# Optimization experiments

Hardware: AMD Instinct MI355X
Metric: run time of the kernel (lower is better)

The kernel has to match this reference:

```python
import jax, jax.numpy as jnp
import numpy as np

B, S, D, H = 4, 1024, 1024, 16
HD = D // H  # head_dim = 64


def setup_inputs() -> dict:
    key = jax.random.key(0)
    ks = jax.random.split(key, 18)
    s = 0.02
    return {
        "x": jax.random.normal(ks[0], (B, S, D), jnp.float32),
        "trust_scores": jax.random.uniform(ks[1], (B, S), jnp.float32),
        "mask": jax.random.randint(ks[2], (B, S), 0, 2).astype(jnp.int32),
        # Linear weights stored as (in, out); torch does x @ W.T + b, equivalent here.
        "Wq": jax.random.normal(ks[3], (D, D), jnp.float32) * s,
        "bq": jnp.zeros((D,), jnp.float32),
        "Wk": jax.random.normal(ks[4], (D, D), jnp.float32) * s,
        "bk": jnp.zeros((D,), jnp.float32),
        "Wv": jax.random.normal(ks[5], (D, D), jnp.float32) * s,
        "bv": jnp.zeros((D,), jnp.float32),
        "Wtp": jax.random.normal(ks[6], (1, HD), jnp.float32) * s,
        "btp": jnp.zeros((HD,), jnp.float32),
        "Wg": jax.random.normal(ks[7], (D + 1, D), jnp.float32) * s,
        "bg": jnp.zeros((D,), jnp.float32),
        "Wo": jax.random.normal(ks[8], (D, D), jnp.float32) * s,
        "bo": jnp.zeros((D,), jnp.float32),
    }


def reference(x, trust_scores, mask, Wq, bq, Wk, bk, Wv, bv, Wtp, btp, Wg, bg, Wo, bo):
    b, s, d = x.shape
    hd = Wtp.shape[1]
    h = d // hd
    # QKV projections -> [b, h, s, hd]
    q = (x @ Wq + bq).reshape(b, s, h, hd).transpose(0, 2, 1, 3)
    k = (x @ Wk + bk).reshape(b, s, h, hd).transpose(0, 2, 1, 3)
    v = (x @ Wv + bv).reshape(b, s, h, hd).transpose(0, 2, 1, 3)
    scores = jnp.einsum("bhqd,bhkd->bhqk", q, k) / jnp.sqrt(jnp.float32(hd))
    # Trust affinity bias: project scalar trust -> head_dim, outer-product + sigmoid.
    trust_proj = trust_scores[:, :, None] @ Wtp + btp  # [b, s, hd]
    trust_aff = jax.nn.sigmoid(jnp.einsum("bqd,bkd->bqk", trust_proj, trust_proj))
    scores = scores + 0.1 * trust_aff[:, None, :, :]  # broadcast over heads
    # Mask applies along the QUERY axis (mask.unsqueeze(1).unsqueeze(-1) in torch).
    scores = jnp.where(mask[:, None, :, None] == 0, jnp.float32(-1e9), scores)
    attn = jax.nn.softmax(scores, axis=-1)  # [b, h, s, s]
    attended = jnp.einsum("bhqk,bhkd->bhqd", attn, v)
    attended = attended.transpose(0, 2, 1, 3).reshape(b, s, d)
    # Trust gate: sigmoid(Linear([attended, trust])) elementwise gate.
    gate_in = jnp.concatenate([attended, trust_scores[:, :, None]], axis=-1)
    gate = jax.nn.sigmoid(gate_in @ Wg + bg)
    attended = attended * gate
    output = attended @ Wo + bo
    return (output, attn)
```

## Files before the change

### kernel.cpp

```cpp
#include <hip/hip_runtime.h>
#include <math.h>

#define BB 4
#define SS 1024
#define DD 1024
#define HH 16
#define HDD 64
#define MTOT (BB*SS)
#define MB (1024*1024)

typedef float  f32x4  __attribute__((ext_vector_type(4)));
typedef __bf16 bf16x8 __attribute__((ext_vector_type(8)));
typedef unsigned short u16;

__device__ __forceinline__ unsigned short f2bf(float f) {
    union { float f; unsigned u; } v; v.f = f;
    unsigned r = v.u + 0x7FFFu + ((v.u >> 16) & 1u);
    return (unsigned short)(r >> 16);
}
__device__ __forceinline__ float bf2f(unsigned short u) {
    union { unsigned u; float f; } v; v.u = ((unsigned)u) << 16;
    return v.f;
}
__device__ __forceinline__ f32x4 mfma16(bf16x8 a, bf16x8 b, f32x4 c) {
    return __builtin_amdgcn_mfma_f32_16x16x32_bf16(a, b, c, 0, 0, 0);
}
__device__ __forceinline__ void gload16(const void* g, void* l) {
    __builtin_amdgcn_global_load_lds(
        (const __attribute__((address_space(1))) void*)g,
        (__attribute__((address_space(3))) void*)l, 16, 0, 0);
}
__device__ __forceinline__ void lds_fence() {
    asm volatile("s_waitcnt lgkmcnt(0)" ::: "memory");
    __builtin_amdgcn_sched_barrier(0);
}

__global__ void split_kernel(const float* __restrict__ in, u16* __restrict__ hi,
                             u16* __restrict__ lo, int n4)
{
    for (int i = blockIdx.x*blockDim.x + threadIdx.x; i < n4; i += gridDim.x*blockDim.x) {
        f32x4 v = ((const f32x4*)in)[i];
        ushort4 h4, l4;
        h4.x = f2bf(v[0]); l4.x = f2bf(v[0] - bf2f(h4.x));
        h4.y = f2bf(v[1]); l4.y = f2bf(v[1] - bf2f(h4.y));
        h4.z = f2bf(v[2]); l4.z = f2bf(v[2] - bf2f(h4.z));
        h4.w = f2bf(v[3]); l4.w = f2bf(v[3] - bf2f(h4.w));
        ((ushort4*)hi)[i] = h4; ((ushort4*)lo)[i] = l4;
    }
}

__global__ __launch_bounds__(256)
void tsplit5_kernel(const float* W0, u16* h0,
                    const float* W1, u16* h1,
                    const float* W2, u16* h2,
                    const float* W3, u16* h3,
                    const float* W4, u16* h4, u16* l4T)
{
    const float* W; u16* hT; u16* lT = nullptr;
    switch (blockIdx.z) {
        case 0: W = W0; hT = h0; break;
        case 1: W = W1; hT = h1; break;
        case 2: W = W2; hT = h2; break;
        case 3: W = W3; hT = h3; break;
        default: W = W4; hT = h4; lT = l4T; break;
    }
    __shared__ float tile[64][65];
    const int t  = threadIdx.x;
    const int k0 = blockIdx.y * 64, n0 = blockIdx.x * 64;
    const int r  = t >> 4, c4 = (t & 15) * 4;
    #pragma unroll
    for (int rr = 0; rr < 4; ++rr) {
        const int k = r + rr*16;
        f32x4 v = *(const f32x4*)&W[(size_t)(k0 + k)*1024 + n0 + c4];
        tile[k][c4+0] = v[0]; tile[k][c4+1] = v[1]; tile[k][c4+2] = v[2]; tile[k][c4+3] = v[3];
    }
    __syncthreads();
    #pragma unroll
    for (int rr = 0; rr < 4; ++rr) {
        const int nl = r + rr*16;
        ushort4 hh, ll;
        {
            float v;
            v = tile[c4+0][nl]; hh.x = f2bf(v); ll.x = f2bf(v - bf2f(hh.x));
            v = tile[c4+1][nl]; hh.y = f2bf(v); ll.y = f2bf(v - bf2f(hh.y));
            v = tile[c4+2][nl]; hh.z = f2bf(v); ll.z = f2bf(v - bf2f(hh.z));
            v = tile[c4+3][nl]; hh.w = f2bf(v); ll.w = f2bf(v - bf2f(hh.w));
        }
        *(ushort4*)&hT[(size_t)(n0 + nl)*1024 + k0 + c4] = hh;
        if (lT) *(ushort4*)&lT[(size_t)(n0 + nl)*1024 + k0 + c4] = ll;
    }
}

__global__ void tconst_kernel(const float* __restrict__ Wtp, const float* __restrict__ btp,
                              float* __restrict__ out3)
{
    const int l = threadIdx.x;
    const float w = Wtp[l], b = btp[l];
    float a = w*w, m = w*b, c = b*b;
    #pragma unroll
    for (int s = 32; s; s >>= 1) {
        a += __shfl_down(a, s);
        m += __shfl_down(m, s);
        c += __shfl_down(c, s);
    }
    if (l == 0) { out3[0] = a; out3[1] = m; out3[2] = c; }
}

__global__ __launch_bounds__(256)
void tbias_kernel(const float* __restrict__ trust, const float* __restrict__ tconst,
                  u16* __restrict__ T)
{
    const int b = blockIdx.y;
    const int q = blockIdx.x;
    const float tq = trust[b*SS + q];
    const float c1 = tconst[0], c2 = tconst[1], c3 = tconst[2];
    const int k0 = threadIdx.x * 4;
    f32x4 tk = *(const f32x4*)&trust[b*SS + k0];
    ushort4 o;
    #pragma unroll
    for (int j = 0; j < 4; ++j) {
        const float ta = c1*tq*tk[j] + c2*(tq + tk[j]) + c3;
        const float v  = 0.1f/(1.f + __expf(-ta));
        ((u16*)&o)[j] = f2bf(v);
    }
    *(ushort4*)&T[((size_t)b*SS + q)*SS + k0] = o;
}

template<int MODE, int PASSES>
__global__ __launch_bounds__(256)
void mgemm(const u16* __restrict__ Ah, const u16* __restrict__ Al,
           const u16* __restrict__ Bh, const u16* __restrict__ Bl,
           const float* __restrict__ bias,
           float* __restrict__ outF, u16* __restrict__ outH, u16* __restrict__ outL,
           int M, int N,
           const float* __restrict__ trust, const float* __restrict__ wlast,
           const u16* __restrict__ attH, const u16* __restrict__ attL)
{
    constexpr int NT   = (PASSES == 3) ? 4 : (PASSES == 2) ? 3 : 2;
    constexpr int BIDX = (PASSES == 1) ? 1 : 2;
    __shared__ u16 lds[2][NT][128*64];

    const int t    = threadIdx.x;
    const int lane = t & 63, wave = t >> 6;
    const int l15  = lane & 15, l4 = lane >> 4;
    const int wr   = wave >> 1, wc = wave & 1;
    const int w64  = wave << 6;
    const int m0   = blockIdx.y * 128, n0 = blockIdx.x * 128;

    const u16* srcs[NT];
    srcs[0] = Ah + (size_t)m0*1024;
    if (PASSES >= 2) srcs[1] = Al + (size_t)m0*1024;
    srcs[BIDX] = Bh + (size_t)n0*1024;
    if (PASSES == 3) srcs[3] = Bl + (size_t)n0*1024;

    f32x4 acc[4][4];
    #pragma unroll
    for (int i = 0; i < 4; ++i)
        #pragma unroll
        for (int j = 0; j < 4; ++j) acc[i][j] = (f32x4){0.f,0.f,0.f,0.f};

#define STAGE(BUF, KOFF) do {                                                  \
    _Pragma("unroll")                                                          \
    for (int tl_ = 0; tl_ < NT; ++tl_) {                                       \
        _Pragma("unroll")                                                      \
        for (int it_ = 0; it_ < 4; ++it_) {                                    \
            const int idx_ = it_*256 + t;                                      \
            const int row_ = idx_ >> 3;                                        \
            const int c_   = (idx_ & 7) ^ (row_ & 7);                          \
            gload16(srcs[tl_] + (KOFF) + (size_t)row_*1024 + c_*8,             \
                    &lds[BUF][tl_][(it_*256 + w64)*8]);                        \
        }                                                                      \
    }                                                                          \
} while(0)

#define COMPUTE(BUF) do {                                                      \
    _Pragma("unroll")                                                          \
    for (int kk_ = 0; kk_ < 2; ++kk_) {                                        \
        const int cb_ = (kk_<<2) + l4;                                         \
        bf16x8 ah_[4], al_[4];                                                 \
        _Pragma("unroll")                                                      \
        for (int i_ = 0; i_ < 4; ++i_) {                                       \
            const int row_ = (wr<<6) + (i_<<4) + l15;                          \
            const int off_ = (row_<<6) + ((cb_ ^ (row_&7)) << 3);              \
            ah_[i_] = *(const bf16x8*)&lds[BUF][0][off_];                      \
            if (PASSES >= 2) al_[i_] = *(const bf16x8*)&lds[BUF][1][off_];     \
        }                                                                      \
        _Pragma("unroll")                                                      \
        for (int j_ = 0; j_ < 4; ++j_) {                                       \
            const int row_ = (wc<<6) + (j_<<4) + l15;                          \
            const int off_ = (row_<<6) + ((cb_ ^ (row_&7)) << 3);              \
            bf16x8 bh_ = *(const bf16x8*)&lds[BUF][BIDX][off_];                \
            bf16x8 bl_;                                                        \
            if (PASSES == 3) bl_ = *(const bf16x8*)&lds[BUF][3][off_];         \
            _Pragma("unroll")                                                  \
            for (int i_ = 0; i_ < 4; ++i_) {                                   \
                acc[i_][j_] = mfma16(ah_[i_], bh_, acc[i_][j_]);               \
                if (PASSES == 3) acc[i_][j_] = mfma16(ah_[i_], bl_, acc[i_][j_]); \
                if (PASSES >= 2) acc[i_][j_] = mfma16(al_[i_], bh_, acc[i_][j_]); \
            }                                                                  \
        }                                                                      \
    }                                                                          \
} while(0)

    STAGE(0, 0);
    __syncthreads();
    int cur = 0;
    for (int s = 0; s < 15; ++s) {
        if (cur == 0) STAGE(1, (s+1)*64);
        else          STAGE(0, (s+1)*64);
        COMPUTE(cur);
        __syncthreads();
        cur ^= 1;
    }
    COMPUTE(cur);
#undef STAGE
#undef COMPUTE

    #pragma unroll
    for (int i = 0; i < 4; ++i)
        #pragma unroll
        for (int j = 0; j < 4; ++j)
            #pragma unroll
            for (int r = 0; r < 4; ++r) {
                const int m = m0 + (wr<<6) + (i<<4) + (l4<<2) + r;
                const int n = n0 + (wc<<6) + (j<<4) + l15;
                const float v = acc[i][j][r];
                if (MODE == 0) {
                    outF[(size_t)m*N + n] = v + bias[n];
                } else if (MODE == 2) {
                    outH[(size_t)m*N + n] = f2bf(v + bias[n]);
                } else if (MODE == 4) {
                    const size_t blk = (((size_t)((m >> 10)*16 + (n >> 6)))*64
                                        + ((m >> 4) & 63))*1024;
                    outH[blk + ((n & 63) >> 3)*128 + (m & 15)*8 + (n & 7)]
                        = f2bf(v + bias[n]);
                } else if (MODE == 5) {
                    const size_t blk = ((((size_t)((n >> 10)*16 + (m >> 6)))*32
                                        + ((n & 1023) >> 5))*4 + ((m & 63) >> 4))*512;
                    outH[blk + ((n & 31) >> 3)*128 + (m & 15)*8 + (n & 7)]
                        = f2bf(v + bias[m]);
                } else {
                    const float pre = v + bias[n] + trust[m]*wlast[n];
                    const float g = 1.f/(1.f + __expf(-pre));
                    const float att = bf2f(attH[(size_t)m*N + n]) + bf2f(attL[(size_t)m*N + n]);
                    const float gated = att*g;
                    const unsigned short hb = f2bf(gated);
                    outH[(size_t)m*N + n] = hb;
                    outL[(size_t)m*N + n] = f2bf(gated - bf2f(hb));
                }
            }
}

__global__ __launch_bounds__(512, 4)
void attn_kernel(const u16* __restrict__ Qb, const u16* __restrict__ Kf,
                 const u16* __restrict__ Vf, const u16* __restrict__ T,
                 const int* __restrict__ mask,
                 float* __restrict__ attnOut, u16* __restrict__ attH, u16* __restrict__ attL)
{
    __shared__ float Pw[8][16*68 + 16];
    __shared__ float redA[8][16];
    __shared__ float redB[8][16];

    const int t    = threadIdx.x;
    const int lane = t & 63, wave = t >> 6;
    const int l15  = lane & 15, l4 = lane >> 4;

    const int bid  = blockIdx.x;
    const int xcd  = bid & 7;
    const int idx0 = bid >> 3;
    const int q0   = (idx0 & 63) * 16;
    const int Pn   = ((idx0 >> 6) << 3) + xcd;
    const int h    = Pn & 15;
    const int b    = Pn >> 4;

    float* myP = Pw[wave];

    int mrow[4];
    #pragma unroll
    for (int r = 0; r < 4; ++r) mrow[r] = mask[b*SS + q0 + l4*4 + r];

    const u16* Qp = Qb + ((size_t)(b*SS + q0 + l15))*DD + h*HDD + l4*8;
    bf16x8 qf0 = *(const bf16x8*)Qp;
    bf16x8 qf1 = *(const bf16x8*)(Qp + 32);

    f32x4 sacc[8];
    #pragma unroll
    for (int tt = 0; tt < 8; ++tt) sacc[tt] = (f32x4){0.f,0.f,0.f,0.f};

    const u16* Kbase = Kf + (((size_t)(b*16 + h))*64 + wave*8)*1024 + l4*128 + l15*8;
    #pragma unroll
    for (int tt = 0; tt < 8; ++tt) {
        bf16x8 kf0 = *(const bf16x8*)(Kbase + tt*1024);
        bf16x8 kf1 = *(const bf16x8*)(Kbase + tt*1024 + 512);
        sacc[tt] = mfma16(qf0, kf0, sacc[tt]);
        sacc[tt] = mfma16(qf1, kf1, sacc[tt]);
    }

    const u16* Tb = T + ((size_t)b*SS + q0 + l4*4)*SS + wave*128 + l15;
    float mx[4] = {-3e38f, -3e38f, -3e38f, -3e38f};
    #pragma unroll
    for (int tt = 0; tt < 8; ++tt) {
        #pragma unroll
        for (int r = 0; r < 4; ++r) {
            const float bias = bf2f(Tb[(size_t)r*SS + tt*16]);
            float s = sacc[tt][r]*0.125f + bias;
            s = mrow[r] ? s : -1e9f;
            sacc[tt][r] = s;
            mx[r] = fmaxf(mx[r], s);
        }
    }
    #pragma unroll
    for (int r = 0; r < 4; ++r)
        #pragma unroll
        for (int xm = 1; xm < 16; xm <<= 1) mx[r] = fmaxf(mx[r], __shfl_xor(mx[r], xm));
    if (l15 == 0) {
        #pragma unroll
        for (int r = 0; r < 4; ++r) redA[wave][l4*4 + r] = mx[r];
    }
    __syncthreads();

    float mxa[4];
    #pragma unroll
    for (int r = 0; r < 4; ++r) {
        const int row = l4*4 + r;
        float m = redA[0][row];
        #pragma unroll
        for (int w = 1; w < 8; ++w) m = fmaxf(m, redA[w][row]);
        mxa[r] = m;
    }

    float sum[4] = {0.f, 0.f, 0.f, 0.f};
    #pragma unroll
    for (int tt = 0; tt < 8; ++tt)
        #pragma unroll
        for (int r = 0; r < 4; ++r) {
            const float p = __expf(sacc[tt][r] - mxa[r]);
            sacc[tt][r] = p;
            sum[r] += p;
        }
    #pragma unroll
    for (int r = 0; r < 4; ++r)
        #pragma unroll
        for (int xm = 1; xm < 16; xm <<= 1) sum[r] += __shfl_xor(sum[r], xm);
    if (l15 == 0) {
        #pragma unroll
        for (int r = 0; r < 4; ++r) redB[wave][l4*4 + r] = sum[r];
    }
    __syncthreads();

    float inv4[4];
    #pragma unroll
    for (int r = 0; r < 4; ++r) {
        const int row = l4*4 + r;
        float s8 = 0.f;
        #pragma unroll
        for (int w = 0; w < 8; ++w) s8 += redB[w][row];
        inv4[r] = 1.f / s8;
    }
    float wiv4[4];
    #pragma unroll
    for (int it = 0; it < 4; ++it) {
        const int row = it*4 + l4;
        float s8 = 0.f;
        #pragma unroll
        for (int w = 0; w < 8; ++w) s8 += redB[w][row];
        wiv4[it] = 1.f / s8;
    }

    float* gBase = attnOut + (((size_t)(b*HH + h))*SS + q0)*SS + wave*128;
    f32x4 pv[4];
    #pragma unroll
    for (int nt = 0; nt < 4; ++nt) pv[nt] = (f32x4){0.f,0.f,0.f,0.f};

    #pragma unroll
    for (int half = 0; half < 2; ++half) {
        #pragma unroll
        for (int t2 = 0; t2 < 4; ++t2)
            #pragma unroll
            for (int r = 0; r < 4; ++r)
                myP[(l4*4 + r)*68 + t2*16 + l15] = sacc[half*4 + t2][r];
        lds_fence();

        #pragma unroll
        for (int it = 0; it < 4; ++it) {
            const int row = it*4 + l4;
            f32x4 v = *(f32x4*)&myP[row*68 + l15*4];
            v *= wiv4[it];
            *(f32x4*)&gBase[(size_t)row*SS + half*64 + l15*4] = v;
        }

        #pragma unroll
        for (int kg = 0; kg < 2; ++kg) {
            const int c0 = kg*32 + l4*8;
            f32x4 a0 = *(f32x4*)&myP[l15*68 + c0];
            f32x4 a1 = *(f32x4*)&myP[l15*68 + c0 + 4];
            bf16x8 af;
            af[0] = (__bf16)a0[0]; af[1] = (__bf16)a0[1]; af[2] = (__bf16)a0[2]; af[3] = (__bf16)a0[3];
            af[4] = (__bf16)a1[0]; af[5] = (__bf16)a1[1]; af[6] = (__bf16)a1[2]; af[7] = (__bf16)a1[3];
            const int kc = wave*4 + half*2 + kg;
            const u16* Vp = Vf + (((size_t)(b*16 + h))*32 + kc)*2048 + l4*128 + l15*8;
            #pragma unroll
            for (int nt = 0; nt < 4; ++nt) {
                bf16x8 bf = *(const bf16x8*)(Vp + nt*512);
                pv[nt] = mfma16(af, bf, pv[nt]);
            }
        }
        lds_fence();
    }

    #pragma unroll
    for (int nt = 0; nt < 4; ++nt)
        #pragma unroll
        for (int r = 0; r < 4; ++r)
            myP[(l4*4 + r)*64 + nt*16 + l15] = pv[nt][r] * inv4[r];
    __syncthreads();

    {
        const int q = t >> 5, d0 = (t & 31)*2;
        float sx = 0.f, sy = 0.f;
        #pragma unroll
        for (int w = 0; w < 8; ++w) {
            float2 v = *(float2*)&Pw[w][q*64 + d0];
            sx += v.x; sy += v.y;
        }
        const size_t off = ((size_t)(b*SS + q0 + q))*DD + h*HDD + d0;
        const unsigned short h0 = f2bf(sx), h1 = f2bf(sy);
        ushort2 hh = {h0, h1};
        ushort2 ll = {f2bf(sx - bf2f(h0)), f2bf(sy - bf2f(h1))};
        *(ushort2*)&attH[off] = hh;
        *(ushort2*)&attL[off] = ll;
    }
}

extern "C" void kernel_launch(void* const* d_in, const int* in_sizes, int n_in,
                              void* d_out, int out_size, void* d_ws, size_t ws_size,
                              hipStream_t stream) {
    const float* x     = (const float*)d_in[0];
    const float* trust = (const float*)d_in[1];
    const int*   mask  = (const int*)  d_in[2];
    const float* Wq    = (const float*)d_in[3];
    const float* bq    = (const float*)d_in[4];
    const float* Wk    = (const float*)d_in[5];
    const float* bk    = (const float*)d_in[6];
    const float* Wv    = (const float*)d_in[7];
    const float* bv    = (const float*)d_in[8];
    const float* Wtp   = (const float*)d_in[9];
    const float* btp   = (const float*)d_in[10];
    const float* Wg    = (const float*)d_in[11];
    const float* bg    = (const float*)d_in[12];
    const float* Wo    = (const float*)d_in[13];
    const float* bo    = (const float*)d_in[14];

    float* out     = (float*)d_out;
    float* attnOut = out + (size_t)MTOT * DD;

    char* ws = (char*)d_ws;
    u16* xh   = (u16*)(ws + (size_t)0*MB);
    u16* xl   = (u16*)(ws + (size_t)8*MB);
    u16* WqTh = (u16*)(ws + (size_t)16*MB);
    u16* WkTh = (u16*)(ws + (size_t)18*MB);
    u16* WvTh = (u16*)(ws + (size_t)20*MB);
    u16* WgTh = (u16*)(ws + (size_t)22*MB);
    u16* WoTh = (u16*)(ws + (size_t)24*MB);
    u16* WoTl = (u16*)(ws + (size_t)26*MB);
    u16* Qbf  = (u16*)(ws + (size_t)28*MB);
    u16* Kfb  = (u16*)(ws + (size_t)36*MB);
    u16* Vfb  = (u16*)(ws + (size_t)44*MB);
    u16* Tb   = (u16*)(ws + (size_t)52*MB);
    float* tconst = (float*)(ws + (size_t)60*MB);
    u16* attH = xh;
    u16* attL = xl;
    u16* Gh   = Qbf;
    u16* Gl   = Kfb;

    const dim3 blk(256);

    tconst_kernel<<<1, 64, 0, stream>>>(Wtp, btp, tconst);
    tbias_kernel<<<dim3(SS, BB), blk, 0, stream>>>(trust, tconst, Tb);
    split_kernel<<<2048, blk, 0, stream>>>(x, xh, xl, MTOT*DD/4);
    tsplit5_kernel<<<dim3(16, 16, 5), blk, 0, stream>>>(
        Wq, WqTh, Wk, WkTh, Wv, WvTh, Wg, WgTh, Wo, WoTh, WoTl);

    mgemm<2,2><<<dim3(DD/128, MTOT/128), blk, 0, stream>>>(
        xh, xl, WqTh, nullptr, bq, nullptr, Qbf, nullptr, MTOT, DD,
        nullptr, nullptr, nullptr, nullptr);
    mgemm<4,2><<<dim3(DD/128, MTOT/128), blk, 0, stream>>>(
        xh, xl, WkTh, nullptr, bk, nullptr, Kfb, nullptr, MTOT, DD,
        nullptr, nullptr, nullptr, nullptr);
    mgemm<5,1><<<dim3(MTOT/128, DD/128), blk, 0, stream>>>(
        WvTh, nullptr, xh, nullptr, bv, nullptr, Vfb, nullptr, DD, MTOT,
        nullptr, nullptr, nullptr, nullptr);

    attn_kernel<<<dim3(4096), dim3(512), 0, stream>>>(
        Qbf, Kfb, Vfb, Tb, mask, attnOut, attH, attL);

    mgemm<1,1><<<dim3(DD/128, MTOT/128), blk, 0, stream>>>(
        attH, nullptr, WgTh, nullptr, bg, nullptr, Gh, Gl, MTOT, DD,
        trust, Wg + (size_t)DD*DD, attH, attL);
    mgemm<0,3><<<dim3(DD/128, MTOT/128), blk, 0, stream>>>(
        Gh, Gl, WoTh, WoTl, bo, out, nullptr, nullptr, MTOT, DD,
        nullptr, nullptr, nullptr, nullptr);
}
```

Baseline: 247.4 us.

## Fuse Q/K projections into one single-pass GEMM and tile trust-bias layout

```diff
diff --git a/kernel.cpp b/kernel.cpp
--- a/kernel.cpp
+++ b/kernel.cpp
@@ -40,12 +40,15 @@
 {
     for (int i = blockIdx.x*blockDim.x + threadIdx.x; i < n4; i += gridDim.x*blockDim.x) {
         f32x4 v = ((const f32x4*)in)[i];
-        ushort4 h4, l4;
-        h4.x = f2bf(v[0]); l4.x = f2bf(v[0] - bf2f(h4.x));
-        h4.y = f2bf(v[1]); l4.y = f2bf(v[1] - bf2f(h4.y));
-        h4.z = f2bf(v[2]); l4.z = f2bf(v[2] - bf2f(h4.z));
-        h4.w = f2bf(v[3]); l4.w = f2bf(v[3] - bf2f(h4.w));
-        ((ushort4*)hi)[i] = h4; ((ushort4*)lo)[i] = l4;
+        ushort4 h4;
+        h4.x = f2bf(v[0]); h4.y = f2bf(v[1]); h4.z = f2bf(v[2]); h4.w = f2bf(v[3]);
+        ((ushort4*)hi)[i] = h4;
+        if (lo) {
+            ushort4 l4v;
+            l4v.x = f2bf(v[0] - bf2f(h4.x)); l4v.y = f2bf(v[1] - bf2f(h4.y));
+            l4v.z = f2bf(v[2] - bf2f(h4.z)); l4v.w = f2bf(v[3] - bf2f(h4.w));
+            ((ushort4*)lo)[i] = l4v;
+        }
     }
 }
 
@@ -108,22 +111,28 @@
 
 __global__ __launch_bounds__(256)
 void tbias_kernel(const float* __restrict__ trust, const float* __restrict__ tconst,
-                  u16* __restrict__ T)
+                  u16* __restrict__ T2)
 {
-    const int b = blockIdx.y;
-    const int q = blockIdx.x;
-    const float tq = trust[b*SS + q];
+    const int qt = blockIdx.x;
+    const int b  = blockIdx.y;
+    const int t  = threadIdx.x;
+    const int lane = t & 63, grp = t >> 6;
+    const int l15 = lane & 15, l4 = lane >> 4;
     const float c1 = tconst[0], c2 = tconst[1], c3 = tconst[2];
-    const int k0 = threadIdx.x * 4;
-    f32x4 tk = *(const f32x4*)&trust[b*SS + k0];
-    ushort4 o;
-    #pragma unroll
-    for (int j = 0; j < 4; ++j) {
-        const float ta = c1*tq*tk[j] + c2*(tq + tk[j]) + c3;
-        const float v  = 0.1f/(1.f + __expf(-ta));
-        ((u16*)&o)[j] = f2bf(v);
-    }
-    *(ushort4*)&T[((size_t)b*SS + q)*SS + k0] = o;
+    float tq[4];
+    #pragma unroll
+    for (int r = 0; r < 4; ++r) tq[r] = trust[b*SS + qt*16 + l4*4 + r];
+    for (int kt2 = 0; kt2 < 16; ++kt2) {
+        const int kt = grp*16 + kt2;
+        const float tk = trust[b*SS + kt*16 + l15];
+        ushort4 o;
+        #pragma unroll
+        for (int r = 0; r < 4; ++r) {
+            const float ta = c1*tq[r]*tk + c2*(tq[r] + tk) + c3;
+            ((u16*)&o)[r] = f2bf(0.1f/(1.f + __expf(-ta)));
+        }
+        *(ushort4*)&T2[((((size_t)b*64 + qt)*64 + kt)*64 + lane)*4] = o;
+    }
 }
 
 template<int MODE, int PASSES>
@@ -150,7 +159,12 @@
     const u16* srcs[NT];
     srcs[0] = Ah + (size_t)m0*1024;
     if (PASSES >= 2) srcs[1] = Al + (size_t)m0*1024;
-    srcs[BIDX] = Bh + (size_t)n0*1024;
+    if (MODE == 6) {
+        srcs[BIDX] = (n0 < 1024) ? Bh + (size_t)n0*1024
+                                 : Bl + (size_t)(n0 - 1024)*1024;
+    } else {
+        srcs[BIDX] = Bh + (size_t)n0*1024;
+    }
     if (PASSES == 3) srcs[3] = Bl + (size_t)n0*1024;
 
     f32x4 acc[4][4];
@@ -239,6 +253,16 @@
                                         + ((n & 1023) >> 5))*4 + ((m & 63) >> 4))*512;
                     outH[blk + ((n & 31) >> 3)*128 + (m & 15)*8 + (n & 7)]
                         = f2bf(v + bias[m]);
+                } else if (MODE == 6) {
+                    if (n0 < 1024) {
+                        outH[(size_t)m*1024 + n] = f2bf(v + bias[n]);
+                    } else {
+                        const int nk = n - 1024;
+                        const size_t blk = (((size_t)((m >> 10)*16 + (nk >> 6)))*64
+                                            + ((m >> 4) & 63))*1024;
+                        outL[blk + ((nk & 63) >> 3)*128 + (m & 15)*8 + (nk & 7)]
+                            = f2bf(v + wlast[nk]);
+                    }
                 } else {
                     const float pre = v + bias[n] + trust[m]*wlast[n];
                     const float g = 1.f/(1.f + __expf(-pre));
@@ -268,10 +292,11 @@
     const int bid  = blockIdx.x;
     const int xcd  = bid & 7;
     const int idx0 = bid >> 3;
-    const int q0   = (idx0 & 63) * 16;
-    const int Pn   = ((idx0 >> 6) << 3) + xcd;
-    const int h    = Pn & 15;
-    const int b    = Pn >> 4;
+    const int p3   = idx0 & 7;
+    const int q6   = idx0 >> 3;
+    const int q0   = q6 * 16;
+    const int b    = xcd >> 1;
+    const int h    = ((xcd & 1) << 3) + p3;
 
     float* myP = Pw[wave];
 
@@ -296,13 +321,14 @@
         sacc[tt] = mfma16(qf1, kf1, sacc[tt]);
     }
 
-    const u16* Tb = T + ((size_t)b*SS + q0 + l4*4)*SS + wave*128 + l15;
+    const u16* Tb = T + ((((size_t)b*64 + q6)*64 + wave*8)*64 + lane)*4;
     float mx[4] = {-3e38f, -3e38f, -3e38f, -3e38f};
     #pragma unroll
     for (int tt = 0; tt < 8; ++tt) {
+        ushort4 t4 = *(const ushort4*)(Tb + (size_t)tt*256);
         #pragma unroll
         for (int r = 0; r < 4; ++r) {
-            const float bias = bf2f(Tb[(size_t)r*SS + tt*16]);
+            const float bias = bf2f(((const u16*)&t4)[r]);
             float s = sacc[tt][r]*0.125f + bias;
             s = mrow[r] ? s : -1e9f;
             sacc[tt][r] = s;
@@ -456,7 +482,7 @@
 
     char* ws = (char*)d_ws;
     u16* xh   = (u16*)(ws + (size_t)0*MB);
-    u16* xl   = (u16*)(ws + (size_t)8*MB);
+    u16* attL = (u16*)(ws + (size_t)8*MB);
     u16* WqTh = (u16*)(ws + (size_t)16*MB);
     u16* WkTh = (u16*)(ws + (size_t)18*MB);
     u16* WvTh = (u16*)(ws + (size_t)20*MB);
@@ -469,24 +495,20 @@
     u16* Tb   = (u16*)(ws + (size_t)52*MB);
     float* tconst = (float*)(ws + (size_t)60*MB);
     u16* attH = xh;
-    u16* attL = xl;
     u16* Gh   = Qbf;
     u16* Gl   = Kfb;
 
     const dim3 blk(256);
 
     tconst_kernel<<<1, 64, 0, stream>>>(Wtp, btp, tconst);
-    tbias_kernel<<<dim3(SS, BB), blk, 0, stream>>>(trust, tconst, Tb);
-    split_kernel<<<2048, blk, 0, stream>>>(x, xh, xl, MTOT*DD/4);
+    tbias_kernel<<<dim3(64, BB), blk, 0, stream>>>(trust, tconst, Tb);
+    split_kernel<<<2048, blk, 0, stream>>>(x, xh, nullptr, MTOT*DD/4);
     tsplit5_kernel<<<dim3(16, 16, 5), blk, 0, stream>>>(
         Wq, WqTh, Wk, WkTh, Wv, WvTh, Wg, WgTh, Wo, WoTh, WoTl);
 
-    mgemm<2,2><<<dim3(DD/128, MTOT/128), blk, 0, stream>>>(
-        xh, xl, WqTh, nullptr, bq, nullptr, Qbf, nullptr, MTOT, DD,
-        nullptr, nullptr, nullptr, nullptr);
-    mgemm<4,2><<<dim3(DD/128, MTOT/128), blk, 0, stream>>>(
-        xh, xl, WkTh, nullptr, bk, nullptr, Kfb, nullptr, MTOT, DD,
-        nullptr, nullptr, nullptr, nullptr);
+    mgemm<6,1><<<dim3(2048/128, MTOT/128), blk, 0, stream>>>(
+        xh, nullptr, WqTh, WkTh, bq, nullptr, Qbf, Kfb, MTOT, 2048,
+        nullptr, bk, nullptr, nullptr);
     mgemm<5,1><<<dim3(MTOT/128, DD/128), blk, 0, stream>>>(
         WvTh, nullptr, xh, nullptr, bv, nullptr, Vfb, nullptr, DD, MTOT,
         nullptr, nullptr, nullptr, nullptr);
```

Result: faster. 241.7 us (-2.3%).
